# Kernel tuning notes

Hardware: AMD Instinct MI355X
Metric: run time of the kernel (lower is better)

Reference implementation:

```python
import jax, jax.numpy as jnp
import numpy as np

N_NODES = 50000
N_EDGES = 1600000
N_GRAPHS = 64
DIMS = [3, 256, 256, 256]  # in -> hidden -> hidden -> output
BN_EPS = 1e-5


def setup_inputs() -> dict:
    key = jax.random.key(0)
    ks = jax.random.split(key, 32)
    inp = {}
    inp['x'] = jax.random.normal(ks[0], (N_NODES, DIMS[0]), dtype=jnp.float32)
    inp['edge_index'] = jax.random.randint(ks[1], (2, N_EDGES), 0, N_NODES, dtype=jnp.int64)
    inp['batch'] = jnp.sort(jax.random.randint(ks[2], (N_NODES,), 0, N_GRAPHS, dtype=jnp.int64))
    k = 3
    for i in range(3):
        fi, fo = DIMS[i], DIMS[i + 1]
        inp[f'W{i}'] = jax.random.normal(ks[k], (fi, fo), dtype=jnp.float32) / np.sqrt(fi); k += 1
        inp[f'b{i}'] = jnp.zeros((fo,), dtype=jnp.float32)
        inp[f'g{i}'] = jnp.ones((fo,), dtype=jnp.float32)       # BN weight
        inp[f'be{i}'] = jnp.zeros((fo,), dtype=jnp.float32)     # BN bias
        inp[f'm{i}'] = 0.1 * jax.random.normal(ks[k], (fo,), dtype=jnp.float32); k += 1  # running mean
        inp[f'v{i}'] = jax.random.uniform(ks[k], (fo,), dtype=jnp.float32) + 0.5; k += 1  # running var
    return inp


def _gcn_norm(edge_index, n_nodes):
    # add self-loops, compute symmetric normalization (PyG GCNConv gcn_norm)
    loops = jnp.arange(n_nodes, dtype=edge_index.dtype)
    src = jnp.concatenate([edge_index[0], loops])
    dst = jnp.concatenate([edge_index[1], loops])
    deg = jax.ops.segment_sum(jnp.ones_like(dst, dtype=jnp.float32), dst, num_segments=n_nodes)
    dinv = jnp.where(deg > 0, jax.lax.rsqrt(deg), 0.0)
    norm = dinv[src] * dinv[dst]  # [E+N]
    return src, dst, norm


def _gcn_conv(x, W, b, src, dst, norm, n_nodes):
    h = x @ W                                 # [N, out]
    msg = h[src] * norm[:, None]              # gather + edge weight
    out = jax.ops.segment_sum(msg, dst, num_segments=n_nodes)  # scatter-add
    return out + b


def _bn_eval(x, g, be, m, v):
    return (x - m) * jax.lax.rsqrt(v + BN_EPS) * g + be


def _denan(x):
    return jnp.where(jnp.isnan(x), 0.0, x)


def reference(x, edge_index, batch,
              W0, b0, g0, be0, m0, v0,
              W1, b1, g1, be1, m1, v1,
              W2, b2, g2, be2, m2, v2):
    n = x.shape[0]
    src, dst, norm = _gcn_norm(edge_index, n)
    params = [(W0, b0, g0, be0, m0, v0), (W1, b1, g1, be1, m1, v1), (W2, b2, g2, be2, m2, v2)]
    h = x
    for i, (W, b, g, be, m, v) in enumerate(params):
        h = _gcn_conv(h, W, b, src, dst, norm, n)
        h = _bn_eval(h, g, be, m, v)
        if i < 2:
            h = jax.nn.relu(h)  # dropout is identity in eval mode
        h = _denan(h)
    # global_mean_pool over batch segments
    sums = jax.ops.segment_sum(h, batch, num_segments=N_GRAPHS)
    cnt = jax.ops.segment_sum(jnp.ones((n,), dtype=h.dtype), batch, num_segments=N_GRAPHS)
    out = sums / jnp.maximum(cnt, 1.0)[:, None]
    return _denan(out)
```

## Files before the change

### kernel.cpp

```cpp
#include <hip/hip_runtime.h>

#define NFEAT 256
#define BN_EPSF 1e-5f
#define CH_J 512
#define ELLW 96
#define BSH 7
#define PBKT 392
#define PCAP 4608
#define PEDG 4992
#define W1_SCALE 8.0f
#define Y_DESCALE 0.125f

typedef __attribute__((ext_vector_type(8))) short bf16x8;
typedef __attribute__((ext_vector_type(4))) float f32x4;
typedef __attribute__((ext_vector_type(2))) float f32x2;

__device__ __forceinline__ unsigned short f2bf(float f) {
    union { float f; unsigned u; } v; v.f = f;
    unsigned r = v.u + 0x7fffu + ((v.u >> 16) & 1u);
    return (unsigned short)(r >> 16);
}
__device__ __forceinline__ float bf2f(unsigned short h) {
    union { unsigned u; float f; } v; v.u = ((unsigned)h) << 16;
    return v.f;
}


__global__ __launch_bounds__(256) void k_part_prep(const int* __restrict__ src, const int* __restrict__ dst,
                                                   int* __restrict__ curD, int* __restrict__ curS,
                                                   unsigned* __restrict__ partD, unsigned* __restrict__ partS,
                                                   int E, int NPB,
                                                   const float* __restrict__ W1,
                                                   unsigned char* __restrict__ Wt_hi, unsigned char* __restrict__ Wt_lo,
                                                   const float* __restrict__ x, float4* __restrict__ x4, int N) {
    __shared__ int cD[PBKT], cS[PBKT], bD[PBKT], bS[PBKT];
    __shared__ int2 eds[PEDG];
    if ((int)blockIdx.x >= NPB) {
        int bx = (int)blockIdx.x - NPB;
        if (bx < 256) {
            int n = bx, k = threadIdx.x;
            float w8 = W1[k * 256 + n] * W1_SCALE;
            int ph = __builtin_amdgcn_cvt_pk_fp8_f32(w8, w8, 0, false);
            f32x2 dec = __builtin_amdgcn_cvt_pk_f32_fp8(ph, false);
            int pl = __builtin_amdgcn_cvt_pk_fp8_f32(w8 - dec[0], w8 - dec[0], 0, false);
            Wt_hi[n * 256 + k] = (unsigned char)(ph & 0xff);
            Wt_lo[n * 256 + k] = (unsigned char)(pl & 0xff);
        } else {
            int i = (bx - 256) * 256 + threadIdx.x;
            if (i < N) {
                float4 r; r.x = x[i * 3 + 0]; r.y = x[i * 3 + 1]; r.z = x[i * 3 + 2]; r.w = 0.f;
                x4[i] = r;
            }
        }
        return;
    }
    for (int t = threadIdx.x; t < PBKT; t += 256) { cD[t] = 0; cS[t] = 0; }
    __syncthreads();
    int e0 = blockIdx.x * PEDG;
    int ne = min(E - e0, PEDG);
    for (int i = threadIdx.x; i < ne; i += 256) {
        int2 e; e.x = src[e0 + i]; e.y = dst[e0 + i];
        eds[i] = e;
        atomicAdd(&cD[e.y >> BSH], 1);
        atomicAdd(&cS[e.x >> BSH], 1);
    }
    __syncthreads();
    for (int t = threadIdx.x; t < PBKT; t += 256) {
        bD[t] = cD[t] ? atomicAdd(&curD[t], cD[t]) : 0;
        bS[t] = cS[t] ? atomicAdd(&curS[t], cS[t]) : 0;
        cD[t] = 0; cS[t] = 0;
    }
    __syncthreads();
    for (int i = threadIdx.x; i < ne; i += 256) {
        int2 e = eds[i];
        int b1 = e.y >> BSH;
        int p1 = bD[b1] + atomicAdd(&cD[b1], 1);
        if (p1 < PCAP) partD[(size_t)b1 * PCAP + p1] = ((unsigned)(e.y & 127) << 16) | (unsigned)e.x;
        int b2 = e.x >> BSH;
        int p2 = bS[b2] + atomicAdd(&cS[b2], 1);
        if (p2 < PCAP) partS[(size_t)b2 * PCAP + p2] = ((unsigned)(e.x & 127) << 16) | (unsigned)e.y;
    }
}

__global__ __launch_bounds__(256) void k_buildIn(const unsigned* __restrict__ partD, const int* __restrict__ curD,
                                                 const int* __restrict__ batch,
                                                 unsigned short* __restrict__ ell_in, int* __restrict__ cnt,
                                                 float* __restrict__ dinv, float2* __restrict__ pack, int N) {
    __shared__ int rows[128][ELLW];
    __shared__ int cur[128];
    int b = blockIdx.x;
    if (threadIdx.x < 128) cur[threadIdx.x] = 0;
    __syncthreads();
    int lo = b << BSH;
    int ne = min(curD[b], PCAP);
    const unsigned* seg = partD + (size_t)b * PCAP;
    for (int i = threadIdx.x; i < ne; i += 256) {
        unsigned u = seg[i];
        int r = u >> 16;
        int pos = atomicAdd(&cur[r], 1);
        if (pos < ELLW) rows[r][pos] = (int)(u & 0xFFFFu);
    }
    __syncthreads();
    const int Q = ELLW / 8;
    for (int idx = threadIdx.x; idx < 128 * Q; idx += 256) {
        int r = idx / Q, q = idx % Q;
        if (lo + r < N) {
            unsigned short tmp[8];
#pragma unroll
            for (int j = 0; j < 8; j++) tmp[j] = (unsigned short)rows[r][q * 8 + j];
            *(uint4*)(ell_in + (size_t)(lo + r) * ELLW + q * 8) = *(const uint4*)tmp;
        }
    }
    if (threadIdx.x < 128) {
        int node = lo + threadIdx.x;
        if (node < N) {
            int c = cur[threadIdx.x];
            cnt[node] = c;
            float d = rsqrtf((float)(min(c, ELLW) + 1));
            dinv[node] = d;
            float2 pk; pk.x = d; pk.y = __int_as_float(batch[node]);
            pack[node] = pk;
        }
    }
}


__global__ __launch_bounds__(256) void k_bct_l0(const unsigned* __restrict__ partS, const int* __restrict__ curS,
                                                const float2* __restrict__ pack,
                                                unsigned short* __restrict__ ct_hi,
                                                unsigned short* __restrict__ ct_lo,
                                                const float4* __restrict__ x4, const unsigned short* __restrict__ ell_in,
                                                const int* __restrict__ cnt, const float* __restrict__ dinv,
                                                const float* __restrict__ W, const float* __restrict__ b,
                                                const float* __restrict__ g, const float* __restrict__ be,
                                                const float* __restrict__ m, const float* __restrict__ v,
                                                unsigned char* __restrict__ h8, int N, int N_pad) {
    __shared__ float ct[128][65];
    __shared__ float dv[128];
    if (blockIdx.x < PBKT) {
        int bq = blockIdx.x;
        for (int idx = threadIdx.x; idx < 128 * 65; idx += 256) (&ct[0][0])[idx] = 0.f;
        __syncthreads();
        int lo = bq << BSH;
        int ne = min(curS[bq], PCAP);
        const unsigned* seg = partS + (size_t)bq * PCAP;
        for (int i = threadIdx.x; i < ne; i += 256) {
            unsigned u = seg[i];
            float2 pk = pack[u & 0xFFFFu];
            atomicAdd(&ct[u >> 16][__float_as_int(pk.y)], pk.x);
        }
        __syncthreads();
        if (threadIdx.x < 128) {
            int node = lo + threadIdx.x;
            if (node < N) {
                float2 ps = pack[node];
                dv[threadIdx.x] = ps.x;
                ct[threadIdx.x][__float_as_int(ps.y)] += ps.x;
            } else dv[threadIdx.x] = 0.f;
        }
        __syncthreads();
        int gq = threadIdx.x >> 2, js = (threadIdx.x & 3) * 32;
        unsigned short hv[32], lv[32];
#pragma unroll
        for (int j = 0; j < 32; j++) {
            float val = dv[js + j] * ct[js + j][gq];
            unsigned short h = f2bf(val);
            hv[j] = h;
            lv[j] = f2bf(val - bf2f(h));
        }
        size_t basep = (size_t)gq * N_pad + lo + js;
#pragma unroll
        for (int j = 0; j < 32; j += 8) {
            *(uint4*)(ct_hi + basep + j) = *(const uint4*)&hv[j];
            *(uint4*)(ct_lo + basep + j) = *(const uint4*)&lv[j];
        }
        return;
    }
    int wv = threadIdx.x >> 6, lane = threadIdx.x & 63;
    int node = ((int)blockIdx.x - PBKT) * 4 + wv;
    int c4 = lane * 4;
    if (node >= N) {
        if (node < N_pad) *(unsigned*)(h8 + (size_t)node * NFEAT + c4) = 0u;
        return;
    }
    float dvn = dinv[node];
    int len = min(cnt[node], ELLW);
    const unsigned short* nb = ell_in + (size_t)node * ELLW;
    float a0 = 0.f, a1 = 0.f, a2 = 0.f;
    for (int e = lane; e < len; e += 64) {
        int s = nb[e];
        float4 xv = x4[s];
        float w = dinv[s] * dvn;
        a0 += w * xv.x;
        a1 += w * xv.y;
        a2 += w * xv.z;
    }
#pragma unroll
    for (int off = 32; off; off >>= 1) {
        a0 += __shfl_xor(a0, off);
        a1 += __shfl_xor(a1, off);
        a2 += __shfl_xor(a2, off);
    }
    float4 xs = x4[node];
    float wself = dvn * dvn;
    a0 += wself * xs.x;
    a1 += wself * xs.y;
    a2 += wself * xs.z;
    float4 w0 = *(const float4*)(W + c4);
    float4 w1 = *(const float4*)(W + NFEAT + c4);
    float4 w2 = *(const float4*)(W + 2 * NFEAT + c4);
    float4 bb = *(const float4*)(b + c4);
    float4 gg = *(const float4*)(g + c4);
    float4 ee = *(const float4*)(be + c4);
    float4 mm = *(const float4*)(m + c4);
    float4 vv = *(const float4*)(v + c4);
    float r0 = ((a0 * w0.x + a1 * w1.x + a2 * w2.x) + bb.x - mm.x) * rsqrtf(vv.x + BN_EPSF) * gg.x + ee.x;
    float r1 = ((a0 * w0.y + a1 * w1.y + a2 * w2.y) + bb.y - mm.y) * rsqrtf(vv.y + BN_EPSF) * gg.y + ee.y;
    float r2 = ((a0 * w0.z + a1 * w1.z + a2 * w2.z) + bb.z - mm.z) * rsqrtf(vv.z + BN_EPSF) * gg.z + ee.z;
    float r3 = ((a0 * w0.w + a1 * w1.w + a2 * w2.w) + bb.w - mm.w) * rsqrtf(vv.w + BN_EPSF) * gg.w + ee.w;
    r0 = fmaxf(r0, 0.f); r1 = fmaxf(r1, 0.f); r2 = fmaxf(r2, 0.f); r3 = fmaxf(r3, 0.f);
    int p01 = __builtin_amdgcn_cvt_pk_fp8_f32(r0, r1, 0, false);
    int p23 = __builtin_amdgcn_cvt_pk_fp8_f32(r2, r3, 0, false);
    unsigned pk = (unsigned)(p01 & 0xffff) | ((unsigned)(p23 & 0xffff) << 16);
    *(unsigned*)(h8 + (size_t)node * NFEAT + c4) = pk;
}


__global__ __launch_bounds__(256) void k_mm_mfma(const unsigned char* __restrict__ A8,
                                                 const unsigned char* __restrict__ Bh,
                                                 const unsigned char* __restrict__ Bl,
                                                 const float* __restrict__ dinv,
                                                 unsigned char* __restrict__ C8, int N) {
    __shared__ __align__(16) unsigned char As[4][128][8];
    __shared__ __align__(16) unsigned char Bhs[4][128][8];
    __shared__ __align__(16) unsigned char Bls[4][128][8];
    int bm = blockIdx.x * 128, bn = blockIdx.y * 128;
    int tid = threadIdx.x;
    int lane = tid & 63, wave = tid >> 6;
    int wm = (wave & 1) * 64, wn = (wave >> 1) * 64;
    int lrow = lane & 15, lk = lane >> 4;
    f32x4 acc[4][4] = {};

    for (int k0 = 0; k0 < 256; k0 += 32) {
#pragma unroll
        for (int i = 0; i < 2; i++) {
            int idx = tid + 256 * i;
            int ch = idx & 3, row = idx >> 2;
            *(uint2*)(&As[ch][row][0])  = *(const uint2*)(A8 + (size_t)(bm + row) * 256 + k0 + ch * 8);
            *(uint2*)(&Bhs[ch][row][0]) = *(const uint2*)(Bh + (size_t)(bn + row) * 256 + k0 + ch * 8);
            *(uint2*)(&Bls[ch][row][0]) = *(const uint2*)(Bl + (size_t)(bn + row) * 256 + k0 + ch * 8);
        }
        __syncthreads();
        long af[4], bh[4], bl[4];
#pragma unroll
        for (int r = 0; r < 4; r++) af[r] = *(const long*)(&As[lk][wm + r * 16 + lrow][0]);
#pragma unroll
        for (int c = 0; c < 4; c++) {
            bh[c] = *(const long*)(&Bhs[lk][wn + c * 16 + lrow][0]);
            bl[c] = *(const long*)(&Bls[lk][wn + c * 16 + lrow][0]);
        }
#pragma unroll
        for (int r = 0; r < 4; r++)
#pragma unroll
            for (int c = 0; c < 4; c++) {
                acc[r][c] = __builtin_amdgcn_mfma_f32_16x16x32_fp8_fp8(af[r], bh[c], acc[r][c], 0, 0, 0);
                acc[r][c] = __builtin_amdgcn_mfma_f32_16x16x32_fp8_fp8(af[r], bl[c], acc[r][c], 0, 0, 0);
            }
        __syncthreads();
    }

#pragma unroll
    for (int r = 0; r < 4; r++) {
#pragma unroll
        for (int reg = 0; reg < 4; reg++) {
            int grow = bm + wm + r * 16 + lk * 4 + reg;
            float dn = (grow < N) ? dinv[grow] : 0.f;
            int p01 = __builtin_amdgcn_cvt_pk_fp8_f32(acc[r][0][reg] * dn, acc[r][1][reg] * dn, 0, false);
            int p23 = __builtin_amdgcn_cvt_pk_fp8_f32(acc[r][2][reg] * dn, acc[r][3][reg] * dn, 0, false);
            size_t base = (size_t)grow * 256 + bn + wn + lrow;
            C8[base]      = (unsigned char)(p01 & 0xff);
            C8[base + 16] = (unsigned char)((p01 >> 8) & 0xff);
            C8[base + 32] = (unsigned char)(p23 & 0xff);
            C8[base + 48] = (unsigned char)((p23 >> 8) & 0xff);
        }
    }
}


template <bool RELU>
__global__ __launch_bounds__(64) void k_agg2(const unsigned char* __restrict__ t,
                                             const unsigned short* __restrict__ ell_in,
                                             const int* __restrict__ cnt,
                                             const float* __restrict__ dinv,
                                             const float* __restrict__ b, const float* __restrict__ g,
                                             const float* __restrict__ be, const float* __restrict__ m,
                                             const float* __restrict__ v, unsigned short* __restrict__ out, int N) {
    __shared__ int s_off[64];
    int node = blockIdx.x;
    int c4 = threadIdx.x * 4;
    if (node >= N) {
        ushort4 z = {0, 0, 0, 0};
        *(ushort4*)(out + (size_t)node * NFEAT + c4) = z;
        return;
    }
    const unsigned char* tp = t;
    f32x2 aLo, aHi;
    {
        unsigned u = *(const unsigned*)(tp + (unsigned)((node << 8) + c4));
        aLo = __builtin_amdgcn_cvt_pk_f32_fp8(u, false);
        aHi = __builtin_amdgcn_cvt_pk_f32_fp8(u, true);
    }
    int len = min(cnt[node], ELLW);
    const unsigned short* nb = ell_in + (size_t)node * ELLW;
    for (int base = 0; base < len; base += 64) {
        int chunk = min(64, len - base);
        if ((int)threadIdx.x < chunk)
            s_off[threadIdx.x] = ((int)nb[base + threadIdx.x]) << 8;
        __syncthreads();
        int j = 0;
        for (; j + 8 <= chunk; j += 8) {
            int o0 = s_off[j + 0], o1 = s_off[j + 1], o2 = s_off[j + 2], o3 = s_off[j + 3];
            int o4 = s_off[j + 4], o5 = s_off[j + 5], o6 = s_off[j + 6], o7 = s_off[j + 7];
            unsigned u0 = *(const unsigned*)(tp + (unsigned)(o0 + c4));
            unsigned u1 = *(const unsigned*)(tp + (unsigned)(o1 + c4));
            unsigned u2 = *(const unsigned*)(tp + (unsigned)(o2 + c4));
            unsigned u3 = *(const unsigned*)(tp + (unsigned)(o3 + c4));
            unsigned u4 = *(const unsigned*)(tp + (unsigned)(o4 + c4));
            unsigned u5 = *(const unsigned*)(tp + (unsigned)(o5 + c4));
            unsigned u6 = *(const unsigned*)(tp + (unsigned)(o6 + c4));
            unsigned u7 = *(const unsigned*)(tp + (unsigned)(o7 + c4));
            aLo = aLo + __builtin_amdgcn_cvt_pk_f32_fp8(u0, false);
            aHi = aHi + __builtin_amdgcn_cvt_pk_f32_fp8(u0, true);
            aLo = aLo + __builtin_amdgcn_cvt_pk_f32_fp8(u1, false);
            aHi = aHi + __builtin_amdgcn_cvt_pk_f32_fp8(u1, true);
            aLo = aLo + __builtin_amdgcn_cvt_pk_f32_fp8(u2, false);
            aHi = aHi + __builtin_amdgcn_cvt_pk_f32_fp8(u2, true);
            aLo = aLo + __builtin_amdgcn_cvt_pk_f32_fp8(u3, false);
            aHi = aHi + __builtin_amdgcn_cvt_pk_f32_fp8(u3, true);
            aLo = aLo + __builtin_amdgcn_cvt_pk_f32_fp8(u4, false);
            aHi = aHi + __builtin_amdgcn_cvt_pk_f32_fp8(u4, true);
            aLo = aLo + __builtin_amdgcn_cvt_pk_f32_fp8(u5, false);
            aHi = aHi + __builtin_amdgcn_cvt_pk_f32_fp8(u5, true);
            aLo = aLo + __builtin_amdgcn_cvt_pk_f32_fp8(u6, false);
            aHi = aHi + __builtin_amdgcn_cvt_pk_f32_fp8(u6, true);
            aLo = aLo + __builtin_amdgcn_cvt_pk_f32_fp8(u7, false);
            aHi = aHi + __builtin_amdgcn_cvt_pk_f32_fp8(u7, true);
        }
        for (; j < chunk; j++) {
            unsigned u = *(const unsigned*)(tp + (unsigned)(s_off[j] + c4));
            aLo = aLo + __builtin_amdgcn_cvt_pk_f32_fp8(u, false);
            aHi = aHi + __builtin_amdgcn_cvt_pk_f32_fp8(u, true);
        }
        __syncthreads();
    }
    float s = dinv[node] * Y_DESCALE;
    float a0 = aLo[0] * s, a1 = aLo[1] * s, a2 = aHi[0] * s, a3 = aHi[1] * s;
    float4 bb = *(const float4*)(b + c4);
    float4 gg = *(const float4*)(g + c4);
    float4 ee = *(const float4*)(be + c4);
    float4 mm = *(const float4*)(m + c4);
    float4 vv = *(const float4*)(v + c4);
    float r0 = (a0 + bb.x - mm.x) * rsqrtf(vv.x + BN_EPSF) * gg.x + ee.x;
    float r1 = (a1 + bb.y - mm.y) * rsqrtf(vv.y + BN_EPSF) * gg.y + ee.y;
    float r2 = (a2 + bb.z - mm.z) * rsqrtf(vv.z + BN_EPSF) * gg.z + ee.z;
    float r3 = (a3 + bb.w - mm.w) * rsqrtf(vv.w + BN_EPSF) * gg.w + ee.w;
    if (RELU) { r0 = fmaxf(r0, 0.f); r1 = fmaxf(r1, 0.f); r2 = fmaxf(r2, 0.f); r3 = fmaxf(r3, 0.f); }
    ushort4 o; o.x = f2bf(r0); o.y = f2bf(r1); o.z = f2bf(r2); o.w = f2bf(r3);
    *(ushort4*)(out + (size_t)node * NFEAT + c4) = o;
}


__global__ __launch_bounds__(256) void k_cgemm(const unsigned short* __restrict__ Y,
                                               const unsigned short* __restrict__ ct_hi,
                                               const unsigned short* __restrict__ ct_lo,
                                               float* __restrict__ P, int N_pad) {
    __shared__ __align__(16) unsigned short s_hi[64 * 40];
    __shared__ __align__(16) unsigned short s_lo[64 * 40];
    int tid = threadIdx.x;
    int lane = tid & 63, wv = tid >> 6;
    int lc = lane & 15, q = lane >> 4;
    int cbase = blockIdx.y * 64 + wv * 16;
    int j0 = blockIdx.x * CH_J;
    int sg = tid >> 2, sj8 = (tid & 3) * 8;
    f32x4 acc[4] = {};

    for (int ks = 0; ks < CH_J; ks += 32) {
        size_t cbs = (size_t)sg * N_pad + j0 + ks + sj8;
        *(uint4*)(&s_hi[sg * 40 + sj8]) = *(const uint4*)(ct_hi + cbs);
        *(uint4*)(&s_lo[sg * 40 + sj8]) = *(const uint4*)(ct_lo + cbs);
        __syncthreads();
        const unsigned short* yp = Y + (size_t)(j0 + ks + q * 8) * 256 + cbase + lc;
        bf16x8 a;
#pragma unroll
        for (int jj = 0; jj < 8; jj++) a[jj] = (short)yp[(size_t)jj * 256];
#pragma unroll
        for (int nt = 0; nt < 4; nt++) {
            bf16x8 bh = *(const bf16x8*)(&s_hi[(nt * 16 + lc) * 40 + q * 8]);
            bf16x8 bl = *(const bf16x8*)(&s_lo[(nt * 16 + lc) * 40 + q * 8]);
            acc[nt] = __builtin_amdgcn_mfma_f32_16x16x32_bf16(a, bh, acc[nt], 0, 0, 0);
            acc[nt] = __builtin_amdgcn_mfma_f32_16x16x32_bf16(a, bl, acc[nt], 0, 0, 0);
        }
        __syncthreads();
    }
    float* pp = P + (size_t)blockIdx.x * 64 * 256;
#pragma unroll
    for (int nt = 0; nt < 4; nt++) {
        int gq = nt * 16 + lc;
        *(f32x4*)(pp + (size_t)gq * 256 + cbase + q * 4) = acc[nt];
    }
}


__global__ __launch_bounds__(256) void k_out(const float* __restrict__ P, int nch,
                                             const float* __restrict__ W2,
                                             const int* __restrict__ batch,
                                             const float* __restrict__ b, const float* __restrict__ gw,
                                             const float* __restrict__ be, const float* __restrict__ m,
                                             const float* __restrict__ v,
                                             float* __restrict__ out, int N) {
    __shared__ float s_pool[256];
    __shared__ int s_cnt;
    int g = blockIdx.x;
    int c = threadIdx.x;
    float acc = 0.f;
    const float* pp = P + (size_t)g * 256 + c;
    for (int ch = 0; ch < nch; ch++) acc += pp[(size_t)ch * 64 * 256];
    s_pool[c] = acc;
    if (threadIdx.x == 0) {
        int lo = 0, hi = N;
        while (lo < hi) { int mid = (lo + hi) >> 1; if (batch[mid] < g) lo = mid + 1; else hi = mid; }
        int st = lo;
        lo = 0; hi = N;
        while (lo < hi) { int mid = (lo + hi) >> 1; if (batch[mid] < g + 1) lo = mid + 1; else hi = mid; }
        s_cnt = lo - st;
    }
    __syncthreads();
    float dot = 0.f;
    for (int k = 0; k < 256; k += 4) {
        float4 pk = *(const float4*)(s_pool + k);
        dot += pk.x * W2[(k + 0) * 256 + c];
        dot += pk.y * W2[(k + 1) * 256 + c];
        dot += pk.z * W2[(k + 2) * 256 + c];
        dot += pk.w * W2[(k + 3) * 256 + c];
    }
    float r = 0.f;
    int cntg = s_cnt;
    if (cntg > 0) {
        float mean = dot / (float)cntg + b[c];
        r = (mean - m[c]) * rsqrtf(v[c] + BN_EPSF) * gw[c] + be[c];
    }
    out[g * 256 + c] = r;
}


static inline size_t align_up(size_t x, size_t a) { return (x + a - 1) & ~(a - 1); }

extern "C" void kernel_launch(void* const* d_in, const int* in_sizes, int n_in,
                              void* d_out, int out_size, void* d_ws, size_t ws_size,
                              hipStream_t stream) {
    const float* x = (const float*)d_in[0];
    const int* edge_index = (const int*)d_in[1];
    const int* batch = (const int*)d_in[2];

    const int N = in_sizes[2];
    const int E = in_sizes[1] / 2;
    const int NCH = (N + CH_J - 1) / CH_J;
    const int N_pad = NCH * CH_J;

    const int* e_src = edge_index;
    const int* e_dst = edge_index + E;

    const float* W[3]; const float* bP[3]; const float* gP[3];
    const float* beP[3]; const float* mP[3]; const float* vP[3];
    for (int i = 0; i < 3; i++) {
        W[i]  = (const float*)d_in[3 + 6 * i + 0];
        bP[i] = (const float*)d_in[3 + 6 * i + 1];
        gP[i] = (const float*)d_in[3 + 6 * i + 2];
        beP[i]= (const float*)d_in[3 + 6 * i + 3];
        mP[i] = (const float*)d_in[3 + 6 * i + 4];
        vP[i] = (const float*)d_in[3 + 6 * i + 5];
    }

    char* ws = (char*)d_ws;
    size_t off = 0;
    auto carve = [&](size_t bytes) { void* p = ws + off; off = align_up(off + bytes, 256); return p; };
    int*   curD     = (int*)  carve((size_t)2 * PBKT * 4);
    int*   curS     = curD + PBKT;
    int*   cnt      = (int*)  carve((size_t)N * 4);
    float* dinv     = (float*)carve((size_t)N * 4);
    float2* pack    = (float2*)carve((size_t)N * 8);
    float4* x4      = (float4*)carve((size_t)N * 16);
    unsigned* partD = (unsigned*)carve((size_t)PBKT * PCAP * 4);
    unsigned* partS = (unsigned*)carve((size_t)PBKT * PCAP * 4);
    unsigned short* ell_in = (unsigned short*)carve((size_t)N * ELLW * 2);
    unsigned short* bufA = (unsigned short*)carve((size_t)N_pad * NFEAT * 2);
    unsigned char*  bufA0 = (unsigned char*)carve((size_t)N_pad * NFEAT);
    unsigned char*  bufY = (unsigned char*)carve((size_t)N_pad * NFEAT);
    unsigned char*  Wt_hi = (unsigned char*)carve((size_t)NFEAT * NFEAT);
    unsigned char*  Wt_lo = (unsigned char*)carve((size_t)NFEAT * NFEAT);
    unsigned short* ct_hi = (unsigned short*)carve((size_t)N_pad * 64 * 2);
    unsigned short* ct_lo = (unsigned short*)carve((size_t)N_pad * 64 * 2);
    float* partials = (float*)carve((size_t)NCH * 64 * 256 * 4);
    (void)ws_size;

    hipMemsetAsync(curD, 0, (size_t)2 * PBKT * 4, stream);

    const int BS = 256;
    const int NPB = (E + PEDG - 1) / PEDG;

    k_part_prep<<<NPB + 256 + (N + BS - 1) / BS, BS, 0, stream>>>(
        e_src, e_dst, curD, curS, partD, partS, E, NPB, W[1], Wt_hi, Wt_lo, x, x4, N);
    k_buildIn<<<PBKT, BS, 0, stream>>>(partD, curD, batch, ell_in, cnt, dinv, pack, N);
    k_bct_l0<<<PBKT + N_pad / 4, BS, 0, stream>>>(partS, curS, pack, ct_hi, ct_lo,
                                                  x4, ell_in, cnt, dinv, W[0],
                                                  bP[0], gP[0], beP[0], mP[0], vP[0], bufA0, N, N_pad);
    dim3 mmGrid((N + 127) / 128, 2);
    k_mm_mfma<<<mmGrid, 256, 0, stream>>>(bufA0, Wt_hi, Wt_lo, dinv, bufY, N);
    k_agg2<true><<<N_pad, 64, 0, stream>>>(bufY, ell_in, cnt, dinv,
                                           bP[1], gP[1], beP[1], mP[1], vP[1], bufA, N);
    dim3 cgGrid(NCH, 4);
    k_cgemm<<<cgGrid, 256, 0, stream>>>(bufA, ct_hi, ct_lo, partials, N_pad);
    k_out<<<64, 256, 0, stream>>>(partials, NCH, W[2], batch, bP[2], gP[2], beP[2], mP[2], vP[2],
                                  (float*)d_out, N);
}
```

Before: 315.2 us.

## Restructure fp8 aggregation so each lane gathers 16 bytes across four neighbor groups

The per-node aggregation kernel now splits the wavefront into four groups of 16 lanes. Each lane loads 16 fp8 features (uint4) per neighbor, and each group handles every fourth neighbor, with the self-loop folded into the neighbor list. Partial sums are combined with cross-lane shuffles, and 16 lanes apply the BN epilogue. Out-of-range padding entries point at row N, so they rely on the mm kernel writing zero rows up to N_pad, which is why its grid now covers N_pad. The aim is fewer, wider gather loads and no per-chunk barriers, at the cost of extra shuffle reduction and a tail that leaves 48 lanes idle.

```diff
diff --git a/kernel.cpp b/kernel.cpp
--- a/kernel.cpp
+++ b/kernel.cpp
@@ -295,78 +295,78 @@
                                              const float* __restrict__ b, const float* __restrict__ g,
                                              const float* __restrict__ be, const float* __restrict__ m,
                                              const float* __restrict__ v, unsigned short* __restrict__ out, int N) {
-    __shared__ int s_off[64];
+    __shared__ int s_off[112];
     int node = blockIdx.x;
-    int c4 = threadIdx.x * 4;
+    int lane = threadIdx.x;
     if (node >= N) {
         ushort4 z = {0, 0, 0, 0};
-        *(ushort4*)(out + (size_t)node * NFEAT + c4) = z;
+        *(ushort4*)(out + (size_t)node * NFEAT + lane * 4) = z;
         return;
     }
-    const unsigned char* tp = t;
-    f32x2 aLo, aHi;
+    int len = min(cnt[node], ELLW);
+    int total = len + 1;
+    int padded = (total + 3) & ~3;
+    const unsigned short* nb = ell_in + (size_t)node * ELLW;
     {
-        unsigned u = *(const unsigned*)(tp + (unsigned)((node << 8) + c4));
-        aLo = __builtin_amdgcn_cvt_pk_f32_fp8(u, false);
-        aHi = __builtin_amdgcn_cvt_pk_f32_fp8(u, true);
-    }
-    int len = min(cnt[node], ELLW);
-    const unsigned short* nb = ell_in + (size_t)node * ELLW;
-    for (int base = 0; base < len; base += 64) {
-        int chunk = min(64, len - base);
-        if ((int)threadIdx.x < chunk)
-            s_off[threadIdx.x] = ((int)nb[base + threadIdx.x]) << 8;
-        __syncthreads();
-        int j = 0;
-        for (; j + 8 <= chunk; j += 8) {
-            int o0 = s_off[j + 0], o1 = s_off[j + 1], o2 = s_off[j + 2], o3 = s_off[j + 3];
-            int o4 = s_off[j + 4], o5 = s_off[j + 5], o6 = s_off[j + 6], o7 = s_off[j + 7];
-            unsigned u0 = *(const unsigned*)(tp + (unsigned)(o0 + c4));
-            unsigned u1 = *(const unsigned*)(tp + (unsigned)(o1 + c4));
-            unsigned u2 = *(const unsigned*)(tp + (unsigned)(o2 + c4));
-            unsigned u3 = *(const unsigned*)(tp + (unsigned)(o3 + c4));
-            unsigned u4 = *(const unsigned*)(tp + (unsigned)(o4 + c4));
-            unsigned u5 = *(const unsigned*)(tp + (unsigned)(o5 + c4));
-            unsigned u6 = *(const unsigned*)(tp + (unsigned)(o6 + c4));
-            unsigned u7 = *(const unsigned*)(tp + (unsigned)(o7 + c4));
-            aLo = aLo + __builtin_amdgcn_cvt_pk_f32_fp8(u0, false);
-            aHi = aHi + __builtin_amdgcn_cvt_pk_f32_fp8(u0, true);
-            aLo = aLo + __builtin_amdgcn_cvt_pk_f32_fp8(u1, false);
-            aHi = aHi + __builtin_amdgcn_cvt_pk_f32_fp8(u1, true);
-            aLo = aLo + __builtin_amdgcn_cvt_pk_f32_fp8(u2, false);
-            aHi = aHi + __builtin_amdgcn_cvt_pk_f32_fp8(u2, true);
-            aLo = aLo + __builtin_amdgcn_cvt_pk_f32_fp8(u3, false);
-            aHi = aHi + __builtin_amdgcn_cvt_pk_f32_fp8(u3, true);
-            aLo = aLo + __builtin_amdgcn_cvt_pk_f32_fp8(u4, false);
-            aHi = aHi + __builtin_amdgcn_cvt_pk_f32_fp8(u4, true);
-            aLo = aLo + __builtin_amdgcn_cvt_pk_f32_fp8(u5, false);
-            aHi = aHi + __builtin_amdgcn_cvt_pk_f32_fp8(u5, true);
-            aLo = aLo + __builtin_amdgcn_cvt_pk_f32_fp8(u6, false);
-            aHi = aHi + __builtin_amdgcn_cvt_pk_f32_fp8(u6, true);
-            aLo = aLo + __builtin_amdgcn_cvt_pk_f32_fp8(u7, false);
-            aHi = aHi + __builtin_amdgcn_cvt_pk_f32_fp8(u7, true);
-        }
-        for (; j < chunk; j++) {
-            unsigned u = *(const unsigned*)(tp + (unsigned)(s_off[j] + c4));
-            aLo = aLo + __builtin_amdgcn_cvt_pk_f32_fp8(u, false);
-            aHi = aHi + __builtin_amdgcn_cvt_pk_f32_fp8(u, true);
-        }
-        __syncthreads();
-    }
-    float s = dinv[node] * Y_DESCALE;
-    float a0 = aLo[0] * s, a1 = aLo[1] * s, a2 = aHi[0] * s, a3 = aHi[1] * s;
-    float4 bb = *(const float4*)(b + c4);
-    float4 gg = *(const float4*)(g + c4);
-    float4 ee = *(const float4*)(be + c4);
-    float4 mm = *(const float4*)(m + c4);
-    float4 vv = *(const float4*)(v + c4);
-    float r0 = (a0 + bb.x - mm.x) * rsqrtf(vv.x + BN_EPSF) * gg.x + ee.x;
-    float r1 = (a1 + bb.y - mm.y) * rsqrtf(vv.y + BN_EPSF) * gg.y + ee.y;
-    float r2 = (a2 + bb.z - mm.z) * rsqrtf(vv.z + BN_EPSF) * gg.z + ee.z;
-    float r3 = (a3 + bb.w - mm.w) * rsqrtf(vv.w + BN_EPSF) * gg.w + ee.w;
-    if (RELU) { r0 = fmaxf(r0, 0.f); r1 = fmaxf(r1, 0.f); r2 = fmaxf(r2, 0.f); r3 = fmaxf(r3, 0.f); }
-    ushort4 o; o.x = f2bf(r0); o.y = f2bf(r1); o.z = f2bf(r2); o.w = f2bf(r3);
-    *(ushort4*)(out + (size_t)node * NFEAT + c4) = o;
+        int e0 = (lane == 0) ? node : ((lane <= len) ? (int)nb[lane - 1] : N);
+        s_off[lane] = e0 << 8;
+        int i1 = lane + 64;
+        if (i1 < padded) {
+            int e1 = (i1 <= len) ? (int)nb[i1 - 1] : N;
+            s_off[i1] = e1 << 8;
+        }
+    }
+    __syncthreads();
+    int grp = lane >> 4;
+    int c16 = (lane & 15) * 16;
+    const int* so = s_off + grp;
+    int nst = padded >> 2;
+    f32x2 acc[8] = {};
+#pragma unroll 8
+    for (int j = 0; j < nst; ++j) {
+        int o = so[j * 4];
+        uint4 u = *(const uint4*)(t + (unsigned)(o + c16));
+        acc[0] = acc[0] + __builtin_amdgcn_cvt_pk_f32_fp8(u.x, false);
+        acc[1] = acc[1] + __builtin_amdgcn_cvt_pk_f32_fp8(u.x, true);
+        acc[2] = acc[2] + __builtin_amdgcn_cvt_pk_f32_fp8(u.y, false);
+        acc[3] = acc[3] + __builtin_amdgcn_cvt_pk_f32_fp8(u.y, true);
+        acc[4] = acc[4] + __builtin_amdgcn_cvt_pk_f32_fp8(u.z, false);
+        acc[5] = acc[5] + __builtin_amdgcn_cvt_pk_f32_fp8(u.z, true);
+        acc[6] = acc[6] + __builtin_amdgcn_cvt_pk_f32_fp8(u.w, false);
+        acc[7] = acc[7] + __builtin_amdgcn_cvt_pk_f32_fp8(u.w, true);
+    }
+#pragma unroll
+    for (int k = 0; k < 8; ++k) {
+        float x0 = acc[k][0], x1 = acc[k][1];
+        x0 += __shfl_xor(x0, 16); x1 += __shfl_xor(x1, 16);
+        x0 += __shfl_xor(x0, 32); x1 += __shfl_xor(x1, 32);
+        acc[k][0] = x0; acc[k][1] = x1;
+    }
+    if (lane < 16) {
+        float s = dinv[node] * Y_DESCALE;
+        int cb = lane * 16;
+        unsigned short ov[16];
+#pragma unroll
+        for (int q = 0; q < 4; ++q) {
+            float4 bb = *(const float4*)(b + cb + q * 4);
+            float4 gg = *(const float4*)(g + cb + q * 4);
+            float4 ee = *(const float4*)(be + cb + q * 4);
+            float4 mm = *(const float4*)(m + cb + q * 4);
+            float4 vv = *(const float4*)(v + cb + q * 4);
+            float a0 = acc[2 * q][0] * s, a1 = acc[2 * q][1] * s;
+            float a2 = acc[2 * q + 1][0] * s, a3 = acc[2 * q + 1][1] * s;
+            float r0 = (a0 + bb.x - mm.x) * rsqrtf(vv.x + BN_EPSF) * gg.x + ee.x;
+            float r1 = (a1 + bb.y - mm.y) * rsqrtf(vv.y + BN_EPSF) * gg.y + ee.y;
+            float r2 = (a2 + bb.z - mm.z) * rsqrtf(vv.z + BN_EPSF) * gg.z + ee.z;
+            float r3 = (a3 + bb.w - mm.w) * rsqrtf(vv.w + BN_EPSF) * gg.w + ee.w;
+            if (RELU) { r0 = fmaxf(r0, 0.f); r1 = fmaxf(r1, 0.f); r2 = fmaxf(r2, 0.f); r3 = fmaxf(r3, 0.f); }
+            ov[q * 4 + 0] = f2bf(r0); ov[q * 4 + 1] = f2bf(r1);
+            ov[q * 4 + 2] = f2bf(r2); ov[q * 4 + 3] = f2bf(r3);
+        }
+        unsigned short* op = out + (size_t)node * NFEAT + cb;
+        *(uint4*)(op)     = *(const uint4*)&ov[0];
+        *(uint4*)(op + 8) = *(const uint4*)&ov[8];
+    }
 }
 
 
@@ -514,7 +514,7 @@
     k_bct_l0<<<PBKT + N_pad / 4, BS, 0, stream>>>(partS, curS, pack, ct_hi, ct_lo,
                                                   x4, ell_in, cnt, dinv, W[0],
                                                   bP[0], gP[0], beP[0], mP[0], vP[0], bufA0, N, N_pad);
-    dim3 mmGrid((N + 127) / 128, 2);
+    dim3 mmGrid(N_pad / 128, 2);
     k_mm_mfma<<<mmGrid, 256, 0, stream>>>(bufA0, Wt_hi, Wt_lo, dinv, bufY, N);
     k_agg2<true><<<N_pad, 64, 0, stream>>>(bufY, ell_in, cnt, dinv,
                                            bP[1], gP[1], beP[1], mP[1], vP[1], bufA, N);
```

Measured after the change: 329.0 us. +4.4%, slower.

## Store GEMM output in 64-column slabs and split aggregation into four column passes

Applied to the files above, without the earlier changes.

The fp8 GEMM output is now written in four column-slab planes of 64 features each (node-major within a slab), so each slab is a compact 64-byte-per-node array. Aggregation runs as a 2D grid (node, slab), where each wave has four 16-lane groups handling different neighbors of one 64-column slice, then reduces across the groups with shuffles. This narrows each pass's gather working set, so a slab fits better in L2, and gives each wave four times more independent gathers in flight. The cost is four times as many blocks, a cross-lane reduction, and padded neighbor slots that read a dummy row N.

```diff
diff --git a/kernel.cpp b/kernel.cpp
--- a/kernel.cpp
+++ b/kernel.cpp
@@ -230,7 +230,7 @@
                                                  const unsigned char* __restrict__ Bh,
                                                  const unsigned char* __restrict__ Bl,
                                                  const float* __restrict__ dinv,
-                                                 unsigned char* __restrict__ C8, int N) {
+                                                 unsigned char* __restrict__ C8, int N, int N_pad) {
     __shared__ __align__(16) unsigned char As[4][128][8];
     __shared__ __align__(16) unsigned char Bhs[4][128][8];
     __shared__ __align__(16) unsigned char Bls[4][128][8];
@@ -269,6 +269,8 @@
         __syncthreads();
     }
 
+    int colbase = bn + wn;
+    size_t slab = (size_t)(colbase >> 6) * (size_t)N_pad * 64;
 #pragma unroll
     for (int r = 0; r < 4; r++) {
 #pragma unroll
@@ -277,7 +279,7 @@
             float dn = (grow < N) ? dinv[grow] : 0.f;
             int p01 = __builtin_amdgcn_cvt_pk_fp8_f32(acc[r][0][reg] * dn, acc[r][1][reg] * dn, 0, false);
             int p23 = __builtin_amdgcn_cvt_pk_fp8_f32(acc[r][2][reg] * dn, acc[r][3][reg] * dn, 0, false);
-            size_t base = (size_t)grow * 256 + bn + wn + lrow;
+            size_t base = slab + (size_t)grow * 64 + lrow;
             C8[base]      = (unsigned char)(p01 & 0xff);
             C8[base + 16] = (unsigned char)((p01 >> 8) & 0xff);
             C8[base + 32] = (unsigned char)(p23 & 0xff);
@@ -288,85 +290,101 @@
 
 
 template <bool RELU>
-__global__ __launch_bounds__(64) void k_agg2(const unsigned char* __restrict__ t,
+__global__ __launch_bounds__(64) void k_agg3(const unsigned char* __restrict__ t,
                                              const unsigned short* __restrict__ ell_in,
                                              const int* __restrict__ cnt,
                                              const float* __restrict__ dinv,
                                              const float* __restrict__ b, const float* __restrict__ g,
                                              const float* __restrict__ be, const float* __restrict__ m,
-                                             const float* __restrict__ v, unsigned short* __restrict__ out, int N) {
-    __shared__ int s_off[64];
+                                             const float* __restrict__ v, unsigned short* __restrict__ out,
+                                             int N, int N_pad) {
+    __shared__ int s_off[112];
     int node = blockIdx.x;
-    int c4 = threadIdx.x * 4;
+    int pass = blockIdx.y;
+    int lane = threadIdx.x;
     if (node >= N) {
-        ushort4 z = {0, 0, 0, 0};
-        *(ushort4*)(out + (size_t)node * NFEAT + c4) = z;
+        if (lane < 16) {
+            ushort4 z = {0, 0, 0, 0};
+            *(ushort4*)(out + (size_t)node * NFEAT + pass * 64 + lane * 4) = z;
+        }
         return;
     }
-    const unsigned char* tp = t;
-    f32x2 aLo, aHi;
+    int len = min(cnt[node], ELLW);
+    int total = len + 1;
+    int padded = (total + 3) & ~3;
+    const unsigned short* nb = ell_in + (size_t)node * ELLW;
     {
-        unsigned u = *(const unsigned*)(tp + (unsigned)((node << 8) + c4));
-        aLo = __builtin_amdgcn_cvt_pk_f32_fp8(u, false);
-        aHi = __builtin_amdgcn_cvt_pk_f32_fp8(u, true);
-    }
-    int len = min(cnt[node], ELLW);
-    const unsigned short* nb = ell_in + (size_t)node * ELLW;
-    for (int base = 0; base < len; base += 64) {
-        int chunk = min(64, len - base);
-        if ((int)threadIdx.x < chunk)
-            s_off[threadIdx.x] = ((int)nb[base + threadIdx.x]) << 8;
-        __syncthreads();
-        int j = 0;
-        for (; j + 8 <= chunk; j += 8) {
-            int o0 = s_off[j + 0], o1 = s_off[j + 1], o2 = s_off[j + 2], o3 = s_off[j + 3];
-            int o4 = s_off[j + 4], o5 = s_off[j + 5], o6 = s_off[j + 6], o7 = s_off[j + 7];
-            unsigned u0 = *(const unsigned*)(tp + (unsigned)(o0 + c4));
-            unsigned u1 = *(const unsigned*)(tp + (unsigned)(o1 + c4));
-            unsigned u2 = *(const unsigned*)(tp + (unsigned)(o2 + c4));
-            unsigned u3 = *(const unsigned*)(tp + (unsigned)(o3 + c4));
-            unsigned u4 = *(const unsigned*)(tp + (unsigned)(o4 + c4));
-            unsigned u5 = *(const unsigned*)(tp + (unsigned)(o5 + c4));
-            unsigned u6 = *(const unsigned*)(tp + (unsigned)(o6 + c4));
-            unsigned u7 = *(const unsigned*)(tp + (unsigned)(o7 + c4));
-            aLo = aLo + __builtin_amdgcn_cvt_pk_f32_fp8(u0, false);
-            aHi = aHi + __builtin_amdgcn_cvt_pk_f32_fp8(u0, true);
-            aLo = aLo + __builtin_amdgcn_cvt_pk_f32_fp8(u1, false);
-            aHi = aHi + __builtin_amdgcn_cvt_pk_f32_fp8(u1, true);
-            aLo = aLo + __builtin_amdgcn_cvt_pk_f32_fp8(u2, false);
-            aHi = aHi + __builtin_amdgcn_cvt_pk_f32_fp8(u2, true);
-            aLo = aLo + __builtin_amdgcn_cvt_pk_f32_fp8(u3, false);
-            aHi = aHi + __builtin_amdgcn_cvt_pk_f32_fp8(u3, true);
-            aLo = aLo + __builtin_amdgcn_cvt_pk_f32_fp8(u4, false);
-            aHi = aHi + __builtin_amdgcn_cvt_pk_f32_fp8(u4, true);
-            aLo = aLo + __builtin_amdgcn_cvt_pk_f32_fp8(u5, false);
-            aHi = aHi + __builtin_amdgcn_cvt_pk_f32_fp8(u5, true);
-            aLo = aLo + __builtin_amdgcn_cvt_pk_f32_fp8(u6, false);
-            aHi = aHi + __builtin_amdgcn_cvt_pk_f32_fp8(u6, true);
-            aLo = aLo + __builtin_amdgcn_cvt_pk_f32_fp8(u7, false);
-            aHi = aHi + __builtin_amdgcn_cvt_pk_f32_fp8(u7, true);
-        }
-        for (; j < chunk; j++) {
-            unsigned u = *(const unsigned*)(tp + (unsigned)(s_off[j] + c4));
-            aLo = aLo + __builtin_amdgcn_cvt_pk_f32_fp8(u, false);
-            aHi = aHi + __builtin_amdgcn_cvt_pk_f32_fp8(u, true);
-        }
-        __syncthreads();
-    }
-    float s = dinv[node] * Y_DESCALE;
-    float a0 = aLo[0] * s, a1 = aLo[1] * s, a2 = aHi[0] * s, a3 = aHi[1] * s;
-    float4 bb = *(const float4*)(b + c4);
-    float4 gg = *(const float4*)(g + c4);
-    float4 ee = *(const float4*)(be + c4);
-    float4 mm = *(const float4*)(m + c4);
-    float4 vv = *(const float4*)(v + c4);
-    float r0 = (a0 + bb.x - mm.x) * rsqrtf(vv.x + BN_EPSF) * gg.x + ee.x;
-    float r1 = (a1 + bb.y - mm.y) * rsqrtf(vv.y + BN_EPSF) * gg.y + ee.y;
-    float r2 = (a2 + bb.z - mm.z) * rsqrtf(vv.z + BN_EPSF) * gg.z + ee.z;
-    float r3 = (a3 + bb.w - mm.w) * rsqrtf(vv.w + BN_EPSF) * gg.w + ee.w;
-    if (RELU) { r0 = fmaxf(r0, 0.f); r1 = fmaxf(r1, 0.f); r2 = fmaxf(r2, 0.f); r3 = fmaxf(r3, 0.f); }
-    ushort4 o; o.x = f2bf(r0); o.y = f2bf(r1); o.z = f2bf(r2); o.w = f2bf(r3);
-    *(ushort4*)(out + (size_t)node * NFEAT + c4) = o;
+        int e0 = (lane == 0) ? node : ((lane <= len) ? (int)nb[lane - 1] : N);
+        s_off[lane] = e0 << 6;
+        int i1 = lane + 64;
+        if (i1 < padded) {
+            int e1 = (i1 <= len) ? (int)nb[i1 - 1] : N;
+            s_off[i1] = e1 << 6;
+        }
+    }
+    __syncthreads();
+    int grp = lane >> 4;
+    const unsigned char* gp = t + (size_t)pass * ((size_t)N_pad * 64) + (unsigned)((lane & 15) * 4);
+    int nst = padded >> 2;
+    f32x2 aLo = {0.f, 0.f}, aHi = {0.f, 0.f};
+    int j = 0;
+    for (; j + 8 <= nst; j += 8) {
+        int o0 = s_off[(j + 0) * 4 + grp], o1 = s_off[(j + 1) * 4 + grp];
+        int o2 = s_off[(j + 2) * 4 + grp], o3 = s_off[(j + 3) * 4 + grp];
+        int o4 = s_off[(j + 4) * 4 + grp], o5 = s_off[(j + 5) * 4 + grp];
+        int o6 = s_off[(j + 6) * 4 + grp], o7 = s_off[(j + 7) * 4 + grp];
+        unsigned u0 = *(const unsigned*)(gp + (unsigned)o0);
+        unsigned u1 = *(const unsigned*)(gp + (unsigned)o1);
+        unsigned u2 = *(const unsigned*)(gp + (unsigned)o2);
+        unsigned u3 = *(const unsigned*)(gp + (unsigned)o3);
+        unsigned u4 = *(const unsigned*)(gp + (unsigned)o4);
+        unsigned u5 = *(const unsigned*)(gp + (unsigned)o5);
+        unsigned u6 = *(const unsigned*)(gp + (unsigned)o6);
+        unsigned u7 = *(const unsigned*)(gp + (unsigned)o7);
+        aLo = aLo + __builtin_amdgcn_cvt_pk_f32_fp8(u0, false);
+        aHi = aHi + __builtin_amdgcn_cvt_pk_f32_fp8(u0, true);
+        aLo = aLo + __builtin_amdgcn_cvt_pk_f32_fp8(u1, false);
+        aHi = aHi + __builtin_amdgcn_cvt_pk_f32_fp8(u1, true);
+        aLo = aLo + __builtin_amdgcn_cvt_pk_f32_fp8(u2, false);
+        aHi = aHi + __builtin_amdgcn_cvt_pk_f32_fp8(u2, true);
+        aLo = aLo + __builtin_amdgcn_cvt_pk_f32_fp8(u3, false);
+        aHi = aHi + __builtin_amdgcn_cvt_pk_f32_fp8(u3, true);
+        aLo = aLo + __builtin_amdgcn_cvt_pk_f32_fp8(u4, false);
+        aHi = aHi + __builtin_amdgcn_cvt_pk_f32_fp8(u4, true);
+        aLo = aLo + __builtin_amdgcn_cvt_pk_f32_fp8(u5, false);
+        aHi = aHi + __builtin_amdgcn_cvt_pk_f32_fp8(u5, true);
+        aLo = aLo + __builtin_amdgcn_cvt_pk_f32_fp8(u6, false);
+        aHi = aHi + __builtin_amdgcn_cvt_pk_f32_fp8(u6, true);
+        aLo = aLo + __builtin_amdgcn_cvt_pk_f32_fp8(u7, false);
+        aHi = aHi + __builtin_amdgcn_cvt_pk_f32_fp8(u7, true);
+    }
+    for (; j < nst; ++j) {
+        int o = s_off[j * 4 + grp];
+        unsigned u = *(const unsigned*)(gp + (unsigned)o);
+        aLo = aLo + __builtin_amdgcn_cvt_pk_f32_fp8(u, false);
+        aHi = aHi + __builtin_amdgcn_cvt_pk_f32_fp8(u, true);
+    }
+    float x0 = aLo[0], x1 = aLo[1], x2 = aHi[0], x3 = aHi[1];
+    x0 += __shfl_xor(x0, 16); x1 += __shfl_xor(x1, 16);
+    x2 += __shfl_xor(x2, 16); x3 += __shfl_xor(x3, 16);
+    x0 += __shfl_xor(x0, 32); x1 += __shfl_xor(x1, 32);
+    x2 += __shfl_xor(x2, 32); x3 += __shfl_xor(x3, 32);
+    if (lane < 16) {
+        float s = dinv[node] * Y_DESCALE;
+        int cb = pass * 64 + lane * 4;
+        float4 bb = *(const float4*)(b + cb);
+        float4 gg = *(const float4*)(g + cb);
+        float4 ee = *(const float4*)(be + cb);
+        float4 mm = *(const float4*)(m + cb);
+        float4 vv = *(const float4*)(v + cb);
+        float r0 = (x0 * s + bb.x - mm.x) * rsqrtf(vv.x + BN_EPSF) * gg.x + ee.x;
+        float r1 = (x1 * s + bb.y - mm.y) * rsqrtf(vv.y + BN_EPSF) * gg.y + ee.y;
+        float r2 = (x2 * s + bb.z - mm.z) * rsqrtf(vv.z + BN_EPSF) * gg.z + ee.z;
+        float r3 = (x3 * s + bb.w - mm.w) * rsqrtf(vv.w + BN_EPSF) * gg.w + ee.w;
+        if (RELU) { r0 = fmaxf(r0, 0.f); r1 = fmaxf(r1, 0.f); r2 = fmaxf(r2, 0.f); r3 = fmaxf(r3, 0.f); }
+        ushort4 o; o.x = f2bf(r0); o.y = f2bf(r1); o.z = f2bf(r2); o.w = f2bf(r3);
+        *(ushort4*)(out + (size_t)node * NFEAT + cb) = o;
+    }
 }
 
 
@@ -514,10 +532,11 @@
     k_bct_l0<<<PBKT + N_pad / 4, BS, 0, stream>>>(partS, curS, pack, ct_hi, ct_lo,
                                                   x4, ell_in, cnt, dinv, W[0],
                                                   bP[0], gP[0], beP[0], mP[0], vP[0], bufA0, N, N_pad);
-    dim3 mmGrid((N + 127) / 128, 2);
-    k_mm_mfma<<<mmGrid, 256, 0, stream>>>(bufA0, Wt_hi, Wt_lo, dinv, bufY, N);
-    k_agg2<true><<<N_pad, 64, 0, stream>>>(bufY, ell_in, cnt, dinv,
-                                           bP[1], gP[1], beP[1], mP[1], vP[1], bufA, N);
+    dim3 mmGrid(N_pad / 128, 2);
+    k_mm_mfma<<<mmGrid, 256, 0, stream>>>(bufA0, Wt_hi, Wt_lo, dinv, bufY, N, N_pad);
+    dim3 aggGrid(N_pad, 4);
+    k_agg3<true><<<aggGrid, 64, 0, stream>>>(bufY, ell_in, cnt, dinv,
+                                             bP[1], gP[1], beP[1], mP[1], vP[1], bufA, N, N_pad);
     dim3 cgGrid(NCH, 4);
     k_cgemm<<<cgGrid, 256, 0, stream>>>(bufA, ct_hi, ct_lo, partials, N_pad);
     k_out<<<64, 256, 0, stream>>>(partials, NCH, W[2], batch, bP[2], gP[2], beP[2], mP[2], vP[2],
```

Result: slower. 340.3 us (+7.9%).
